# Kernel tuning notes

Hardware: AMD Instinct MI355X
Metric: run time of the kernel (lower is better)

Reference implementation:

```python
import jax, jax.numpy as jnp
import numpy as np

HEADS = 4
DIM_HEAD = 32


def _ln(x, g, b, eps=1e-5):
    m = x.mean(-1, keepdims=True)
    v = ((x - m) ** 2).mean(-1, keepdims=True)
    return (x - m) * jax.lax.rsqrt(v + eps) * g + b


def setup_inputs() -> dict:
    key = jax.random.key(0)
    B, N, D, H, W, h, w = 2, 6, 128, 50, 50, 14, 30
    HD = HEADS * DIM_HEAD  # 128
    ks = jax.random.split(key, 12)
    inp = {
        'q': jax.random.normal(ks[0], (B, N, D, H, W), jnp.float32),
        'k': jax.random.normal(ks[1], (B, N, D, h, w), jnp.float32),
        'v': jax.random.normal(ks[2], (B, N, D, h, w), jnp.float32),
        'skip': jax.random.normal(ks[3], (B, D, H, W), jnp.float32),
        # to_q / to_k / to_v: LayerNorm(dim) + Linear(dim, heads*dim_head)
        'lnq_g': jnp.ones((D,), jnp.float32), 'lnq_b': jnp.zeros((D,), jnp.float32),
        'wq': jax.random.normal(ks[4], (D, HD), jnp.float32) * 0.02,
        'bq': jnp.zeros((HD,), jnp.float32),
        'lnk_g': jnp.ones((D,), jnp.float32), 'lnk_b': jnp.zeros((D,), jnp.float32),
        'wk': jax.random.normal(ks[5], (D, HD), jnp.float32) * 0.02,
        'bk': jnp.zeros((HD,), jnp.float32),
        'lnv_g': jnp.ones((D,), jnp.float32), 'lnv_b': jnp.zeros((D,), jnp.float32),
        'wv': jax.random.normal(ks[6], (D, HD), jnp.float32) * 0.02,
        'bv': jnp.zeros((HD,), jnp.float32),
        # proj: Linear(heads*dim_head, dim)
        'wp': jax.random.normal(ks[7], (HD, D), jnp.float32) * 0.02,
        'bp': jnp.zeros((D,), jnp.float32),
        # prenorm
        'ln1_g': jnp.ones((D,), jnp.float32), 'ln1_b': jnp.zeros((D,), jnp.float32),
        # mlp: Linear(dim, 2*dim), GELU, Linear(2*dim, dim)
        'w1': jax.random.normal(ks[8], (D, 2 * D), jnp.float32) * 0.02,
        'b1': jnp.zeros((2 * D,), jnp.float32),
        'w2': jax.random.normal(ks[9], (2 * D, D), jnp.float32) * 0.02,
        'b2': jnp.zeros((D,), jnp.float32),
        # postnorm
        'ln2_g': jnp.ones((D,), jnp.float32), 'ln2_b': jnp.zeros((D,), jnp.float32),
    }
    return inp


def reference(q, k, v, skip,
              lnq_g, lnq_b, wq, bq,
              lnk_g, lnk_b, wk, bk,
              lnv_g, lnv_b, wv, bv,
              wp, bp, ln1_g, ln1_b,
              w1, b1, w2, b2, ln2_g, ln2_b):
    B, N, D, H, W = q.shape
    hk = k.shape[3] * k.shape[4]  # keys per camera
    Q = H * W
    M, DH = HEADS, DIM_HEAD
    scale = DH ** -0.5

    # (b n d H W) -> (b n Q d); (b n d h w) -> (b n K d); v -> (b (n K) d)
    qf = q.reshape(B, N, D, Q).transpose(0, 1, 3, 2)
    kf = k.reshape(B, N, D, hk).transpose(0, 1, 3, 2)
    vf = v.reshape(B, N, D, hk).transpose(0, 1, 3, 2).reshape(B, N * hk, D)

    qp = _ln(qf, lnq_g, lnq_b) @ wq + bq          # (B,N,Q,M*DH)
    kp = _ln(kf, lnk_g, lnk_b) @ wk + bk          # (B,N,K,M*DH)
    vp = _ln(vf, lnv_g, lnv_b) @ wv + bv          # (B,N*K,M*DH)

    qh = qp.reshape(B, N, Q, M, DH)
    kh = kp.reshape(B, N, hk, M, DH)
    vh = vp.reshape(B, N * hk, M, DH)

    # In the torch code only dot1+dot2 (queries from cameras 0 and 1) reach the
    # softmax; the q[:,1:]=... writes are no-ops and dot3..dot6 are unused.
    qsum = qh[:, 0] + qh[:, 1]                    # (B,Q,M,DH)
    dot = scale * jnp.einsum('bqmd,bnkmd->bmqnk', qsum, kh)  # (B,M,Q,N,K)
    dot = dot.reshape(B, M, Q, N * hk)
    att = jax.nn.softmax(dot, axis=-1)

    a = jnp.einsum('bmqk,bkmd->bqmd', att, vh).reshape(B, Q, M * DH)
    z = a @ wp + bp                               # (B,Q,D)
    z = z + skip.reshape(B, D, Q).transpose(0, 2, 1)
    z = _ln(z, ln1_g, ln1_b)
    z = z + (jax.nn.gelu(z @ w1 + b1, approximate=False) @ w2 + b2)
    z = _ln(z, ln2_g, ln2_b)
    return z.transpose(0, 2, 1).reshape(B, D, H, W)
```

## Files before the change

### kernel.cpp

```cpp
#include <hip/hip_runtime.h>
#include <hip/hip_bf16.h>
#include <math.h>

#define B_  2
#define N_  6
#define D_  128
#define Q_  2500
#define HK  420
#define NK  2520
#define NKP 2560
#define M_  4
#define DH  32
#define SPLIT 8
#define KPSP 320
#define CHUNKS 10
#define SCALE 0.25503487775f

typedef __attribute__((ext_vector_type(8))) short short8v;
typedef __attribute__((ext_vector_type(4))) float f32x4;
typedef __attribute__((ext_vector_type(2))) unsigned u32x2;
typedef __attribute__((ext_vector_type(4))) unsigned u32x4;

__device__ __forceinline__ unsigned short f2b(float x) {
  unsigned u = __float_as_uint(x);
  return (unsigned short)((u + 0x7FFFu + ((u >> 16) & 1u)) >> 16);
}

__device__ __forceinline__ unsigned pk2(float lo, float hi) {
  return (unsigned)f2b(lo) | ((unsigned)f2b(hi) << 16);
}

__device__ __forceinline__ float bl(unsigned u) { return __uint_as_float(u << 16); }
__device__ __forceinline__ float bh(unsigned u) { return __uint_as_float(u & 0xffff0000u); }

__device__ __forceinline__ int kperm(int a) {
  const int h = a & 7;
  return ((h >= 4) ? 16 : 0) + 4 * (a >> 3) + (h & 3);
}

__global__ __launch_bounds__(256)
void setup_kernel(const float* __restrict__ wp, const float* __restrict__ w1,
                  const float* __restrict__ w2, const float* __restrict__ wq,
                  const float* __restrict__ wk, const float* __restrict__ wv,
                  unsigned short* __restrict__ wpk, unsigned short* __restrict__ w1k,
                  unsigned short* __restrict__ w2k, unsigned short* __restrict__ wqk,
                  unsigned short* __restrict__ wkk, unsigned short* __restrict__ wvk,
                  unsigned short* __restrict__ kpb, unsigned short* __restrict__ vtb)
{
  if (blockIdx.x < 128) {
    const int base = blockIdx.x * 1024 + threadIdx.x * 4;
    #pragma unroll
    for (int i = 0; i < 4; ++i) {
      const int tid = base + i;
      if (tid < 16384) {
        const int e = tid & 7, l = (tid >> 3) & 63, j = (tid >> 9) & 7, c = tid >> 12;
        wpk[tid] = f2b(wp[(32*c + 8*(l>>4) + e) * 128 + 16*j + (l & 15)]);
      } else if (tid < 49152) {
        const int t2 = tid - 16384;
        const int e = t2 & 7, l = (t2 >> 3) & 63, j = (t2 >> 9) & 15, c = t2 >> 13;
        w1k[t2] = f2b(w1[(32*c + 8*(l>>4) + e) * 256 + 16*j + (l & 15)]);
      } else if (tid < 81920) {
        const int t2 = tid - 49152;
        const int e = t2 & 7, l = (t2 >> 3) & 63, j = (t2 >> 9) & 7, c = t2 >> 12;
        w2k[t2] = f2b(w2[(32*c + 8*(l>>4) + e) * 128 + 16*j + (l & 15)]);
      } else {
        const int t2 = (tid - 81920) & 16383;
        const int which = (tid - 81920) >> 14;
        const float* src = which == 0 ? wq : which == 1 ? wk : wv;
        unsigned short* dst = which == 0 ? wqk : which == 1 ? wkk : wvk;
        const int e = t2 & 7, l = (t2 >> 3) & 63, j = (t2 >> 9) & 7, c = t2 >> 12;
        dst[t2] = f2b(src[(32*c + 8*(l>>4) + e) * 128 + 16*j + (l & 15)]);
      }
    }
  } else {
    const int base = (blockIdx.x - 128) * 256 + threadIdx.x;
    for (int i = base; i < 16384; i += 512) {
      const int bm = i >> 11, rem = i & 2047;
      kpb[((size_t)bm * NKP + 2496 + (rem >> 5)) * DH + (rem & 31)] = 0;
      vtb[((size_t)(i >> 6)) * NKP + 2496 + (i & 63)] = 0;
    }
  }
}

__global__ __launch_bounds__(256)
void proj_kernel(const float* __restrict__ kin, const float* __restrict__ vin,
                 const float* __restrict__ lnk_g, const float* __restrict__ lnk_b,
                 const unsigned short* __restrict__ wkk, const float* __restrict__ bk,
                 const float* __restrict__ lnv_g, const float* __restrict__ lnv_b,
                 const unsigned short* __restrict__ wvk, const float* __restrict__ bv,
                 unsigned short* __restrict__ kpb, unsigned short* __restrict__ vtb,
                 const float* __restrict__ qin,
                 const float* __restrict__ lnq_g, const float* __restrict__ lnq_b,
                 const unsigned short* __restrict__ wqk, const float* __restrict__ bq,
                 unsigned short* __restrict__ qsb)
{
  const int wid = threadIdx.x >> 6, lane = threadIdx.x & 63;
  const int l15 = lane & 15, g = lane >> 4;

  if (blockIdx.x < 158) {
    const int T = blockIdx.x * 4 + wid;
    if (T >= 630) return;
    const int ph = T >= 315 ? 1 : 0;
    const int t = ph ? T - 315 : T;

    const float* in = ph ? vin : kin;
    const float* gg = ph ? lnv_g : lnk_g;
    const float* bb = ph ? lnv_b : lnk_b;
    const unsigned short* wf = ph ? wvk : wkk;
    const float* bs = ph ? bv : bk;

    const int myrow = 16 * t + l15;
    const int cam = myrow / HK, kk = myrow - cam * HK;

    float x[4][8];
    float s = 0.f, s2 = 0.f;
    #pragma unroll
    for (int c = 0; c < 4; ++c)
      #pragma unroll
      for (int e = 0; e < 8; ++e) {
        const float xv = in[((size_t)(cam * D_ + 32 * c + 8 * g + e)) * HK + kk];
        x[c][e] = xv; s += xv; s2 += xv * xv;
      }
    s  += __shfl_xor(s, 16);  s2 += __shfl_xor(s2, 16);
    s  += __shfl_xor(s, 32);  s2 += __shfl_xor(s2, 32);
    const float mean = s * (1.f / 128.f);
    const float rstd = rsqrtf(s2 * (1.f / 128.f) - mean * mean + 1e-5f);

    short8v aA[4];
    #pragma unroll
    for (int c = 0; c < 4; ++c)
      #pragma unroll
      for (int e = 0; e < 8; ++e) {
        const int col = 32 * c + 8 * g + e;
        aA[c][e] = (short)f2b((x[c][e] - mean) * rstd * gg[col] + bb[col]);
      }

    f32x4 z[8];
    #pragma unroll
    for (int j = 0; j < 8; ++j) {
      f32x4 d = {0.f, 0.f, 0.f, 0.f};
      #pragma unroll
      for (int c = 0; c < 4; ++c) {
        const short8v w8 = *(const short8v*)(wf + (((c * 8 + j) * 64 + lane) << 3));
        d = __builtin_amdgcn_mfma_f32_16x16x32_bf16(aA[c], w8, d, 0, 0, 0);
      }
      z[j] = d;
    }

    const int key0 = 16 * t + 4 * g;
    #pragma unroll
    for (int j = 0; j < 8; ++j) {
      const int col = 16 * j + l15;
      const float bsv = bs[col];
      if (ph == 0) {
        const int m = col >> 5, dh = col & 31;
        #pragma unroll
        for (int r = 0; r < 4; ++r) {
          const int key = key0 + r;
          const int bbx = key / NK, kb = key - bbx * NK;
          const int kbp = (kb & ~31) | kperm(kb & 31);
          kpb[((size_t)(bbx * M_ + m) * NKP + kbp) * DH + dh] = f2b(z[j][r] + bsv);
        }
      } else {
        #pragma unroll
        for (int r = 0; r < 4; ++r) {
          const int key = key0 + r;
          const int bbx = key / NK, kb = key - bbx * NK;
          vtb[((size_t)(bbx * 128 + col)) * NKP + kb] = f2b(z[j][r] + bsv);
        }
      }
    }
  } else {
    const int t = (blockIdx.x - 158) * 4 + wid;
    if (t >= 313) return;
    int myrow = 16 * t + l15; if (myrow > 4999) myrow = 4999;
    const int b = myrow / Q_, qpos = myrow - b * Q_;

    float xs[4][8];
    #pragma unroll
    for (int c = 0; c < 4; ++c)
      #pragma unroll
      for (int e = 0; e < 8; ++e) xs[c][e] = 0.f;

    #pragma unroll
    for (int n = 0; n < 2; ++n) {
      float x[4][8];
      float s = 0.f, s2 = 0.f;
      #pragma unroll
      for (int c = 0; c < 4; ++c)
        #pragma unroll
        for (int e = 0; e < 8; ++e) {
          const float xv = qin[((size_t)((b * N_ + n) * D_ + 32 * c + 8 * g + e)) * Q_ + qpos];
          x[c][e] = xv; s += xv; s2 += xv * xv;
        }
      s  += __shfl_xor(s, 16);  s2 += __shfl_xor(s2, 16);
      s  += __shfl_xor(s, 32);  s2 += __shfl_xor(s2, 32);
      const float mean = s * (1.f / 128.f);
      const float rstd = rsqrtf(s2 * (1.f / 128.f) - mean * mean + 1e-5f);
      #pragma unroll
      for (int c = 0; c < 4; ++c)
        #pragma unroll
        for (int e = 0; e < 8; ++e) xs[c][e] += (x[c][e] - mean) * rstd;
    }

    short8v aA[4];
    #pragma unroll
    for (int c = 0; c < 4; ++c) {
      #pragma unroll
      for (int e = 0; e < 8; ++e) {
        const int col = 32 * c + 8 * g + e;
        aA[c][e] = (short)f2b(SCALE * (xs[c][e] * lnq_g[col] + 2.f * lnq_b[col]));
      }
    }

    f32x4 z[8];
    #pragma unroll
    for (int j = 0; j < 8; ++j) {
      f32x4 d = {0.f, 0.f, 0.f, 0.f};
      #pragma unroll
      for (int c = 0; c < 4; ++c) {
        const short8v w8 = *(const short8v*)(wqk + (((c * 8 + j) * 64 + lane) << 3));
        d = __builtin_amdgcn_mfma_f32_16x16x32_bf16(aA[c], w8, d, 0, 0, 0);
      }
      z[j] = d;
    }

    const int row0 = 16 * t + 4 * g;
    #pragma unroll
    for (int j = 0; j < 8; ++j) {
      const int col = 16 * j + l15;
      const float bsv = 2.f * SCALE * bq[col];
      #pragma unroll
      for (int r = 0; r < 4; ++r) {
        const int row = row0 + r;
        if (row < 5000) qsb[((size_t)row) * 128 + col] = f2b(z[j][r] + bsv);
      }
    }
  }
}

__global__ __launch_bounds__(256)
void attn_kernel(const unsigned short* __restrict__ qsb,
                 const unsigned short* __restrict__ kpb,
                 const unsigned short* __restrict__ vtb,
                 float* __restrict__ pl, unsigned short* __restrict__ pacc)
{
  const int wid  = threadIdx.x >> 6;
  const int lane = threadIdx.x & 63;
  const int bi = blockIdx.x;
  const int sp = bi & 7;
  const int tmp = bi >> 3;
  const int qg = tmp % 20;
  const int bm = tmp / 20;
  const int qp = qg * 4 + wid;

  const int q16 = lane & 15, g = lane >> 4;
  const int qa = (2 * qp) * 16 + q16;
  const int qb = (2 * qp + 1) * 16 + q16;
  const int qca = qa < Q_ ? qa : Q_ - 1;
  const int qcb = qb < Q_ ? qb : Q_ - 1;
  const int b = bm >> 2;

  const short8v qf0 = *(const short8v*)(qsb + ((size_t)(b * Q_ + qca)) * 128 + (bm & 3) * DH + g * 8);
  const short8v qf1 = *(const short8v*)(qsb + ((size_t)(b * Q_ + qcb)) * 128 + (bm & 3) * DH + g * 8);

  const unsigned short* kbase = kpb + ((size_t)bm * NKP + sp * KPSP) * DH + q16 * DH + g * 8;
  const unsigned short* vbase = vtb + ((size_t)(bm * DH + q16)) * NKP + sp * KPSP + g * 8;

  f32x4 o0a = {0,0,0,0}, o1a = {0,0,0,0}, o0b = {0,0,0,0}, o1b = {0,0,0,0};
  float la = 0.f, lb = 0.f;

  const int c0 = qp % CHUNKS;
  int c1 = c0 + 1; if (c1 >= CHUNKS) c1 -= CHUNKS;
  int cn = c0 + 2; if (cn >= CHUNKS) cn -= CHUNKS;

  short8v kA1 = *(const short8v*)(kbase + c0 * 1024);
  short8v kA2 = *(const short8v*)(kbase + c0 * 1024 + 512);
  short8v vA1 = *(const short8v*)(vbase + c0 * 32);
  short8v vA2 = *(const short8v*)(vbase + c0 * 32 + 16 * NKP);
  short8v kB1 = *(const short8v*)(kbase + c1 * 1024);
  short8v kB2 = *(const short8v*)(kbase + c1 * 1024 + 512);
  short8v vB1 = *(const short8v*)(vbase + c1 * 32);
  short8v vB2 = *(const short8v*)(vbase + c1 * 32 + 16 * NKP);

  auto step = [&](short8v& K1r, short8v& K2r, short8v& V1r, short8v& V2r, int cnx) {
    f32x4 s0a = __builtin_amdgcn_mfma_f32_16x16x32_bf16(K1r, qf0, (f32x4){0.f,0.f,0.f,0.f}, 0, 0, 0);
    f32x4 s1a = __builtin_amdgcn_mfma_f32_16x16x32_bf16(K2r, qf0, (f32x4){0.f,0.f,0.f,0.f}, 0, 0, 0);
    f32x4 s0b = __builtin_amdgcn_mfma_f32_16x16x32_bf16(K1r, qf1, (f32x4){0.f,0.f,0.f,0.f}, 0, 0, 0);
    f32x4 s1b = __builtin_amdgcn_mfma_f32_16x16x32_bf16(K2r, qf1, (f32x4){0.f,0.f,0.f,0.f}, 0, 0, 0);

    float pa[8], pb_[8];
    #pragma unroll
    for (int r = 0; r < 4; ++r) {
      pa[r] = __builtin_amdgcn_exp2f(s0a[r]);  pa[4 + r] = __builtin_amdgcn_exp2f(s1a[r]);
      pb_[r] = __builtin_amdgcn_exp2f(s0b[r]); pb_[4 + r] = __builtin_amdgcn_exp2f(s1b[r]);
    }
    #pragma unroll
    for (int i = 0; i < 8; ++i) { la += pa[i]; lb += pb_[i]; }

    short8v fa, fb;
    #pragma unroll
    for (int i = 0; i < 8; ++i) { fa[i] = (short)f2b(pa[i]); fb[i] = (short)f2b(pb_[i]); }

    o0a = __builtin_amdgcn_mfma_f32_16x16x32_bf16(V1r, fa, o0a, 0, 0, 0);
    o1a = __builtin_amdgcn_mfma_f32_16x16x32_bf16(V2r, fa, o1a, 0, 0, 0);
    o0b = __builtin_amdgcn_mfma_f32_16x16x32_bf16(V1r, fb, o0b, 0, 0, 0);
    o1b = __builtin_amdgcn_mfma_f32_16x16x32_bf16(V2r, fb, o1b, 0, 0, 0);

    K1r = *(const short8v*)(kbase + cnx * 1024);
    K2r = *(const short8v*)(kbase + cnx * 1024 + 512);
    V1r = *(const short8v*)(vbase + cnx * 32);
    V2r = *(const short8v*)(vbase + cnx * 32 + 16 * NKP);
  };

  #pragma unroll 1
  for (int it = 0; it < CHUNKS / 2; ++it) {
    step(kA1, kA2, vA1, vA2, cn);
    cn = cn + 1 >= CHUNKS ? cn + 1 - CHUNKS : cn + 1;
    step(kB1, kB2, vB1, vB2, cn);
    cn = cn + 1 >= CHUNKS ? cn + 1 - CHUNKS : cn + 1;
  }

  la += __shfl_xor(la, 16);  la += __shfl_xor(la, 32);
  lb += __shfl_xor(lb, 16);  lb += __shfl_xor(lb, 32);

  if (qa < Q_) {
    const size_t row = (size_t)(bm * SPLIT + sp) * Q_ + qa;
    if (lane < 16) __builtin_nontemporal_store(la, &pl[row]);
    u32x2 w0, w1;
    w0[0] = pk2(o0a[0], o0a[1]); w0[1] = pk2(o0a[2], o0a[3]);
    w1[0] = pk2(o1a[0], o1a[1]); w1[1] = pk2(o1a[2], o1a[3]);
    __builtin_nontemporal_store(w0, (u32x2*)(pacc + row * DH + 4 * g));
    __builtin_nontemporal_store(w1, (u32x2*)(pacc + row * DH + 16 + 4 * g));
  }
  if (qb < Q_) {
    const size_t row = (size_t)(bm * SPLIT + sp) * Q_ + qb;
    if (lane < 16) __builtin_nontemporal_store(lb, &pl[row]);
    u32x2 w0, w1;
    w0[0] = pk2(o0b[0], o0b[1]); w0[1] = pk2(o0b[2], o0b[3]);
    w1[0] = pk2(o1b[0], o1b[1]); w1[1] = pk2(o1b[2], o1b[3]);
    __builtin_nontemporal_store(w0, (u32x2*)(pacc + row * DH + 4 * g));
    __builtin_nontemporal_store(w1, (u32x2*)(pacc + row * DH + 16 + 4 * g));
  }
}

__global__ __launch_bounds__(256)
void tail_kernel(const float* __restrict__ pl, const unsigned short* __restrict__ pacc,
                 const float* __restrict__ skip,
                 const unsigned short* __restrict__ wpk, const float* __restrict__ bp,
                 const float* __restrict__ ln1_g, const float* __restrict__ ln1_b,
                 const unsigned short* __restrict__ w1k, const float* __restrict__ b1,
                 const unsigned short* __restrict__ w2k, const float* __restrict__ b2,
                 const float* __restrict__ ln2_g, const float* __restrict__ ln2_b,
                 float* __restrict__ out)
{
  __shared__ __align__(16) unsigned short aL[16][136];
  __shared__ __align__(16) unsigned short zl[16][136];
  __shared__ __align__(16) unsigned short hl[16][264];
  __shared__ __align__(16) float stat1[4][16][2];
  __shared__ __align__(16) float stat2[4][16][2];

  const int wid = threadIdx.x >> 6, lane = threadIdx.x & 63;
  const int l15 = lane & 15, g = lane >> 4;
  const int row0 = blockIdx.x * 16;
  const int grow0 = row0 + 4 * g;

  {
    int arow = row0 + l15; if (arow > 4999) arow = 4999;
    const int bb = arow / Q_, qq = arow - bb * Q_;
    float ls = -40.0f;
    float4 a0 = {0,0,0,0}, a1 = {0,0,0,0};
    #pragma unroll
    for (int sp = 0; sp < SPLIT; ++sp) {
      const size_t row = (size_t)((bb * 4 + wid) * SPLIT + sp) * Q_ + qq;
      ls += __builtin_nontemporal_load(&pl[row]);
      const u32x4 t = __builtin_nontemporal_load((const u32x4*)(pacc + row * DH + 8 * g));
      a0.x += bl(t[0]); a0.y += bh(t[0]); a0.z += bl(t[1]); a0.w += bh(t[1]);
      a1.x += bl(t[2]); a1.y += bh(t[2]); a1.z += bl(t[3]); a1.w += bh(t[3]);
    }
    const float inv = 1.f / ls;
    u32x4 w;
    w[0] = pk2(a0.x * inv, a0.y * inv);
    w[1] = pk2(a0.z * inv, a0.w * inv);
    w[2] = pk2(a1.x * inv, a1.y * inv);
    w[3] = pk2(a1.z * inv, a1.w * inv);
    *(u32x4*)&aL[l15][32 * wid + 8 * g] = w;
  }
  __syncthreads();

  short8v aA[4];
  #pragma unroll
  for (int c = 0; c < 4; ++c)
    aA[c] = *(const short8v*)&aL[l15][32 * c + 8 * g];

  f32x4 zres[2];
  #pragma unroll
  for (int jj = 0; jj < 2; ++jj) {
    const int j = 2 * wid + jj;
    f32x4 d = {0.f, 0.f, 0.f, 0.f};
    #pragma unroll
    for (int c = 0; c < 4; ++c) {
      const short8v wf = *(const short8v*)(wpk + (((c * 8 + j) * 64 + lane) << 3));
      d = __builtin_amdgcn_mfma_f32_16x16x32_bf16(aA[c], wf, d, 0, 0, 0);
    }
    zres[jj] = d;
  }

  #pragma unroll
  for (int jj = 0; jj < 2; ++jj) {
    const int col = 16 * (2 * wid + jj) + l15;
    const float bpv = bp[col];
    #pragma unroll
    for (int r = 0; r < 4; ++r) {
      int rr = grow0 + r; if (rr > 4999) rr = 4999;
      const int bb = rr / 2500, q = rr - bb * 2500;
      zres[jj][r] += bpv + skip[((size_t)(bb * 128 + col)) * 2500 + q];
    }
  }

  {
    float sum[4], sq[4];
    #pragma unroll
    for (int r = 0; r < 4; ++r) {
      sum[r] = zres[0][r] + zres[1][r];
      sq[r]  = zres[0][r] * zres[0][r] + zres[1][r] * zres[1][r];
    }
    #pragma unroll
    for (int r = 0; r < 4; ++r) {
      #pragma unroll
      for (int off = 1; off < 16; off <<= 1) {
        sum[r] += __shfl_xor(sum[r], off);
        sq[r]  += __shfl_xor(sq[r], off);
      }
    }
    if (l15 == 0) {
      float4 s0 = {sum[0], sq[0], sum[1], sq[1]};
      float4 s1 = {sum[2], sq[2], sum[3], sq[3]};
      *(float4*)&stat1[wid][4 * g][0]     = s0;
      *(float4*)&stat1[wid][4 * g + 2][0] = s1;
    }
  }
  __syncthreads();

  float mean[4], rstd[4];
  #pragma unroll
  for (int r = 0; r < 4; ++r) {
    float S = 0.f, S2 = 0.f;
    #pragma unroll
    for (int w2 = 0; w2 < 4; ++w2) {
      S  += stat1[w2][4 * g + r][0];
      S2 += stat1[w2][4 * g + r][1];
    }
    mean[r] = S * (1.f / 128.f);
    rstd[r] = rsqrtf(S2 * (1.f / 128.f) - mean[r] * mean[r] + 1e-5f);
  }

  #pragma unroll
  for (int jj = 0; jj < 2; ++jj) {
    const int col = 16 * (2 * wid + jj) + l15;
    const float g1 = ln1_g[col], bv1 = ln1_b[col];
    #pragma unroll
    for (int r = 0; r < 4; ++r) {
      const float vv = (zres[jj][r] - mean[r]) * rstd[r] * g1 + bv1;
      zres[jj][r] = vv;
      zl[4 * g + r][col] = f2b(vv);
    }
  }
  __syncthreads();

  short8v zA[4];
  #pragma unroll
  for (int c = 0; c < 4; ++c)
    zA[c] = *(const short8v*)&zl[l15][32 * c + 8 * g];
  #pragma unroll
  for (int jj = 0; jj < 4; ++jj) {
    const int j = 4 * wid + jj;
    f32x4 d = {0.f, 0.f, 0.f, 0.f};
    #pragma unroll
    for (int c = 0; c < 4; ++c) {
      const short8v wf = *(const short8v*)(w1k + (((c * 16 + j) * 64 + lane) << 3));
      d = __builtin_amdgcn_mfma_f32_16x16x32_bf16(zA[c], wf, d, 0, 0, 0);
    }
    const int col = 16 * j + l15;
    const float bv = b1[col];
    #pragma unroll
    for (int r = 0; r < 4; ++r) {
      const float x = d[r] + bv;
      hl[4 * g + r][col] = f2b(0.5f * x * (1.f + erff(x * 0.70710678118654752f)));
    }
  }
  __syncthreads();

  short8v hA[8];
  #pragma unroll
  for (int c = 0; c < 8; ++c)
    hA[c] = *(const short8v*)&hl[l15][32 * c + 8 * g];
  #pragma unroll
  for (int jj = 0; jj < 2; ++jj) {
    const int j = 2 * wid + jj;
    f32x4 d = {0.f, 0.f, 0.f, 0.f};
    #pragma unroll
    for (int c = 0; c < 8; ++c) {
      const short8v wf = *(const short8v*)(w2k + (((c * 8 + j) * 64 + lane) << 3));
      d = __builtin_amdgcn_mfma_f32_16x16x32_bf16(hA[c], wf, d, 0, 0, 0);
    }
    const int col = 16 * j + l15;
    const float bv = b2[col];
    #pragma unroll
    for (int r = 0; r < 4; ++r) zres[jj][r] += d[r] + bv;
  }

  {
    float sum[4], sq[4];
    #pragma unroll
    for (int r = 0; r < 4; ++r) {
      sum[r] = zres[0][r] + zres[1][r];
      sq[r]  = zres[0][r] * zres[0][r] + zres[1][r] * zres[1][r];
    }
    #pragma unroll
    for (int r = 0; r < 4; ++r) {
      #pragma unroll
      for (int off = 1; off < 16; off <<= 1) {
        sum[r] += __shfl_xor(sum[r], off);
        sq[r]  += __shfl_xor(sq[r], off);
      }
    }
    if (l15 == 0) {
      float4 s0 = {sum[0], sq[0], sum[1], sq[1]};
      float4 s1 = {sum[2], sq[2], sum[3], sq[3]};
      *(float4*)&stat2[wid][4 * g][0]     = s0;
      *(float4*)&stat2[wid][4 * g + 2][0] = s1;
    }
  }
  __syncthreads();

  float mean2[4], rstd2[4];
  #pragma unroll
  for (int r = 0; r < 4; ++r) {
    float S = 0.f, S2 = 0.f;
    #pragma unroll
    for (int w2 = 0; w2 < 4; ++w2) {
      S  += stat2[w2][4 * g + r][0];
      S2 += stat2[w2][4 * g + r][1];
    }
    mean2[r] = S * (1.f / 128.f);
    rstd2[r] = rsqrtf(S2 * (1.f / 128.f) - mean2[r] * mean2[r] + 1e-5f);
  }

  if (grow0 + 3 <= 4999) {
    const int bb = grow0 / 2500, q0 = grow0 - bb * 2500;
    #pragma unroll
    for (int jj = 0; jj < 2; ++jj) {
      const int col = 16 * (2 * wid + jj) + l15;
      const float g2 = ln2_g[col], bv2 = ln2_b[col];
      float4 o;
      o.x = (zres[jj][0] - mean2[0]) * rstd2[0] * g2 + bv2;
      o.y = (zres[jj][1] - mean2[1]) * rstd2[1] * g2 + bv2;
      o.z = (zres[jj][2] - mean2[2]) * rstd2[2] * g2 + bv2;
      o.w = (zres[jj][3] - mean2[3]) * rstd2[3] * g2 + bv2;
      *(float4*)(out + ((size_t)(bb * 128 + col)) * 2500 + q0) = o;
    }
  }
}

extern "C" void kernel_launch(void* const* d_in, const int* in_sizes, int n_in,
                              void* d_out, int out_size, void* d_ws, size_t ws_size,
                              hipStream_t stream)
{
  const float* q     = (const float*)d_in[0];
  const float* k     = (const float*)d_in[1];
  const float* v     = (const float*)d_in[2];
  const float* skip  = (const float*)d_in[3];
  const float* lnq_g = (const float*)d_in[4];
  const float* lnq_b = (const float*)d_in[5];
  const float* wq    = (const float*)d_in[6];
  const float* bq    = (const float*)d_in[7];
  const float* lnk_g = (const float*)d_in[8];
  const float* lnk_b = (const float*)d_in[9];
  const float* wk    = (const float*)d_in[10];
  const float* bk    = (const float*)d_in[11];
  const float* lnv_g = (const float*)d_in[12];
  const float* lnv_b = (const float*)d_in[13];
  const float* wv    = (const float*)d_in[14];
  const float* bv    = (const float*)d_in[15];
  const float* wp    = (const float*)d_in[16];
  const float* bp    = (const float*)d_in[17];
  const float* ln1_g = (const float*)d_in[18];
  const float* ln1_b = (const float*)d_in[19];
  const float* w1    = (const float*)d_in[20];
  const float* b1    = (const float*)d_in[21];
  const float* w2    = (const float*)d_in[22];
  const float* b2    = (const float*)d_in[23];
  const float* ln2_g = (const float*)d_in[24];
  const float* ln2_b = (const float*)d_in[25];

  unsigned short* kpb = (unsigned short*)d_ws;
  unsigned short* vtb = kpb + 655360;
  unsigned short* qsb = vtb + 655360;
  unsigned short* wpk = qsb + 640000;
  unsigned short* w1k = wpk + 16384;
  unsigned short* w2k = w1k + 32768;
  unsigned short* wqk = w2k + 32768;
  unsigned short* wkk = wqk + 16384;
  unsigned short* wvk = wkk + 16384;
  float* pl = (float*)(wvk + 16384);
  unsigned short* pacc = (unsigned short*)(pl + 160000);

  setup_kernel<<<dim3(130), dim3(256), 0, stream>>>(wp, w1, w2, wq, wk, wv,
                                                    wpk, w1k, w2k, wqk, wkk, wvk,
                                                    kpb, vtb);
  proj_kernel<<<dim3(237), dim3(256), 0, stream>>>(
      k, v, lnk_g, lnk_b, wkk, bk, lnv_g, lnv_b, wvk, bv, kpb, vtb,
      q, lnq_g, lnq_b, wqk, bq, qsb);
  attn_kernel<<<dim3(1280), dim3(256), 0, stream>>>(qsb, kpb, vtb, pl, pacc);
  tail_kernel<<<dim3(313), dim3(256), 0, stream>>>(
      pl, pacc, skip, wpk, bp, ln1_g, ln1_b, w1k, b1, w2k, b2, ln2_g, ln2_b, (float*)d_out);
}
```

Measured before the change: 63.21 us.

## Process four query tiles per wave in attention to reuse K/V registers

Each wave in the attention kernel now handles four 16-query tiles instead of two, so every K and V fragment loaded from memory feeds twice as many MFMAs, and the grid is halved to match. The exp/pack step is also restructured to pack probability pairs straight into bf16 words and to issue the next K loads earlier within the step. The aim is to cut redundant K/V global loads per query. In exchange, register pressure rises with eight accumulators and four Q fragments, and there are fewer blocks to fill the GPU.

```diff
diff --git a/kernel.cpp b/kernel.cpp
--- a/kernel.cpp
+++ b/kernel.cpp
@@ -250,27 +250,39 @@
   const int bi = blockIdx.x;
   const int sp = bi & 7;
   const int tmp = bi >> 3;
-  const int qg = tmp % 20;
-  const int bm = tmp / 20;
-  const int qp = qg * 4 + wid;
+  const int qqg = tmp % 10;
+  const int bm = tmp / 10;
+  const int quad = qqg * 4 + wid;
 
   const int q16 = lane & 15, g = lane >> 4;
-  const int qa = (2 * qp) * 16 + q16;
-  const int qb = (2 * qp + 1) * 16 + q16;
-  const int qca = qa < Q_ ? qa : Q_ - 1;
-  const int qcb = qb < Q_ ? qb : Q_ - 1;
   const int b = bm >> 2;
 
-  const short8v qf0 = *(const short8v*)(qsb + ((size_t)(b * Q_ + qca)) * 128 + (bm & 3) * DH + g * 8);
-  const short8v qf1 = *(const short8v*)(qsb + ((size_t)(b * Q_ + qcb)) * 128 + (bm & 3) * DH + g * 8);
+  int qx[4];
+  short8v qf0, qf1, qf2, qf3;
+  {
+    #pragma unroll
+    for (int i = 0; i < 4; ++i) qx[i] = (4 * quad + i) * 16 + q16;
+    const int c0i = qx[0] < Q_ ? qx[0] : Q_ - 1;
+    const int c1i = qx[1] < Q_ ? qx[1] : Q_ - 1;
+    const int c2i = qx[2] < Q_ ? qx[2] : Q_ - 1;
+    const int c3i = qx[3] < Q_ ? qx[3] : Q_ - 1;
+    const size_t off = (bm & 3) * DH + g * 8;
+    qf0 = *(const short8v*)(qsb + ((size_t)(b * Q_ + c0i)) * 128 + off);
+    qf1 = *(const short8v*)(qsb + ((size_t)(b * Q_ + c1i)) * 128 + off);
+    qf2 = *(const short8v*)(qsb + ((size_t)(b * Q_ + c2i)) * 128 + off);
+    qf3 = *(const short8v*)(qsb + ((size_t)(b * Q_ + c3i)) * 128 + off);
+  }
 
   const unsigned short* kbase = kpb + ((size_t)bm * NKP + sp * KPSP) * DH + q16 * DH + g * 8;
   const unsigned short* vbase = vtb + ((size_t)(bm * DH + q16)) * NKP + sp * KPSP + g * 8;
 
-  f32x4 o0a = {0,0,0,0}, o1a = {0,0,0,0}, o0b = {0,0,0,0}, o1b = {0,0,0,0};
-  float la = 0.f, lb = 0.f;
-
-  const int c0 = qp % CHUNKS;
+  f32x4 o0_0 = {0,0,0,0}, o1_0 = {0,0,0,0};
+  f32x4 o0_1 = {0,0,0,0}, o1_1 = {0,0,0,0};
+  f32x4 o0_2 = {0,0,0,0}, o1_2 = {0,0,0,0};
+  f32x4 o0_3 = {0,0,0,0}, o1_3 = {0,0,0,0};
+  float l0 = 0.f, l1 = 0.f, l2 = 0.f, l3 = 0.f;
+
+  const int c0 = quad % CHUNKS;
   int c1 = c0 + 1; if (c1 >= CHUNKS) c1 -= CHUNKS;
   int cn = c0 + 2; if (cn >= CHUNKS) cn -= CHUNKS;
 
@@ -284,31 +296,50 @@
   short8v vB2 = *(const short8v*)(vbase + c1 * 32 + 16 * NKP);
 
   auto step = [&](short8v& K1r, short8v& K2r, short8v& V1r, short8v& V2r, int cnx) {
-    f32x4 s0a = __builtin_amdgcn_mfma_f32_16x16x32_bf16(K1r, qf0, (f32x4){0.f,0.f,0.f,0.f}, 0, 0, 0);
-    f32x4 s1a = __builtin_amdgcn_mfma_f32_16x16x32_bf16(K2r, qf0, (f32x4){0.f,0.f,0.f,0.f}, 0, 0, 0);
-    f32x4 s0b = __builtin_amdgcn_mfma_f32_16x16x32_bf16(K1r, qf1, (f32x4){0.f,0.f,0.f,0.f}, 0, 0, 0);
-    f32x4 s1b = __builtin_amdgcn_mfma_f32_16x16x32_bf16(K2r, qf1, (f32x4){0.f,0.f,0.f,0.f}, 0, 0, 0);
-
-    float pa[8], pb_[8];
-    #pragma unroll
-    for (int r = 0; r < 4; ++r) {
-      pa[r] = __builtin_amdgcn_exp2f(s0a[r]);  pa[4 + r] = __builtin_amdgcn_exp2f(s1a[r]);
-      pb_[r] = __builtin_amdgcn_exp2f(s0b[r]); pb_[4 + r] = __builtin_amdgcn_exp2f(s1b[r]);
-    }
-    #pragma unroll
-    for (int i = 0; i < 8; ++i) { la += pa[i]; lb += pb_[i]; }
-
-    short8v fa, fb;
-    #pragma unroll
-    for (int i = 0; i < 8; ++i) { fa[i] = (short)f2b(pa[i]); fb[i] = (short)f2b(pb_[i]); }
-
-    o0a = __builtin_amdgcn_mfma_f32_16x16x32_bf16(V1r, fa, o0a, 0, 0, 0);
-    o1a = __builtin_amdgcn_mfma_f32_16x16x32_bf16(V2r, fa, o1a, 0, 0, 0);
-    o0b = __builtin_amdgcn_mfma_f32_16x16x32_bf16(V1r, fb, o0b, 0, 0, 0);
-    o1b = __builtin_amdgcn_mfma_f32_16x16x32_bf16(V2r, fb, o1b, 0, 0, 0);
+    f32x4 s0_0 = __builtin_amdgcn_mfma_f32_16x16x32_bf16(K1r, qf0, (f32x4){0.f,0.f,0.f,0.f}, 0, 0, 0);
+    f32x4 s1_0 = __builtin_amdgcn_mfma_f32_16x16x32_bf16(K2r, qf0, (f32x4){0.f,0.f,0.f,0.f}, 0, 0, 0);
+    f32x4 s0_1 = __builtin_amdgcn_mfma_f32_16x16x32_bf16(K1r, qf1, (f32x4){0.f,0.f,0.f,0.f}, 0, 0, 0);
+    f32x4 s1_1 = __builtin_amdgcn_mfma_f32_16x16x32_bf16(K2r, qf1, (f32x4){0.f,0.f,0.f,0.f}, 0, 0, 0);
+    f32x4 s0_2 = __builtin_amdgcn_mfma_f32_16x16x32_bf16(K1r, qf2, (f32x4){0.f,0.f,0.f,0.f}, 0, 0, 0);
+    f32x4 s1_2 = __builtin_amdgcn_mfma_f32_16x16x32_bf16(K2r, qf2, (f32x4){0.f,0.f,0.f,0.f}, 0, 0, 0);
+    f32x4 s0_3 = __builtin_amdgcn_mfma_f32_16x16x32_bf16(K1r, qf3, (f32x4){0.f,0.f,0.f,0.f}, 0, 0, 0);
+    f32x4 s1_3 = __builtin_amdgcn_mfma_f32_16x16x32_bf16(K2r, qf3, (f32x4){0.f,0.f,0.f,0.f}, 0, 0, 0);
 
     K1r = *(const short8v*)(kbase + cnx * 1024);
     K2r = *(const short8v*)(kbase + cnx * 1024 + 512);
+
+    u32x4 u0, u1, u2, u3;
+    float p0, p1;
+    #pragma unroll
+    for (int j = 0; j < 4; ++j) {
+      const int r0 = 2 * j, r1 = 2 * j + 1;
+      const float a0 = __builtin_amdgcn_exp2f(j < 2 ? s0_0[r0] : s1_0[r0 - 4]);
+      const float a1 = __builtin_amdgcn_exp2f(j < 2 ? s0_0[r1] : s1_0[r1 - 4]);
+      l0 += a0 + a1; u0[j] = pk2(a0, a1);
+      const float b0 = __builtin_amdgcn_exp2f(j < 2 ? s0_1[r0] : s1_1[r0 - 4]);
+      const float b1 = __builtin_amdgcn_exp2f(j < 2 ? s0_1[r1] : s1_1[r1 - 4]);
+      l1 += b0 + b1; u1[j] = pk2(b0, b1);
+      const float cc0 = __builtin_amdgcn_exp2f(j < 2 ? s0_2[r0] : s1_2[r0 - 4]);
+      const float cc1 = __builtin_amdgcn_exp2f(j < 2 ? s0_2[r1] : s1_2[r1 - 4]);
+      l2 += cc0 + cc1; u2[j] = pk2(cc0, cc1);
+      const float d0 = __builtin_amdgcn_exp2f(j < 2 ? s0_3[r0] : s1_3[r0 - 4]);
+      const float d1 = __builtin_amdgcn_exp2f(j < 2 ? s0_3[r1] : s1_3[r1 - 4]);
+      l3 += d0 + d1; u3[j] = pk2(d0, d1);
+    }
+    const short8v f0 = __builtin_bit_cast(short8v, u0);
+    const short8v f1 = __builtin_bit_cast(short8v, u1);
+    const short8v f2 = __builtin_bit_cast(short8v, u2);
+    const short8v f3 = __builtin_bit_cast(short8v, u3);
+
+    o0_0 = __builtin_amdgcn_mfma_f32_16x16x32_bf16(V1r, f0, o0_0, 0, 0, 0);
+    o1_0 = __builtin_amdgcn_mfma_f32_16x16x32_bf16(V2r, f0, o1_0, 0, 0, 0);
+    o0_1 = __builtin_amdgcn_mfma_f32_16x16x32_bf16(V1r, f1, o0_1, 0, 0, 0);
+    o1_1 = __builtin_amdgcn_mfma_f32_16x16x32_bf16(V2r, f1, o1_1, 0, 0, 0);
+    o0_2 = __builtin_amdgcn_mfma_f32_16x16x32_bf16(V1r, f2, o0_2, 0, 0, 0);
+    o1_2 = __builtin_amdgcn_mfma_f32_16x16x32_bf16(V2r, f2, o1_2, 0, 0, 0);
+    o0_3 = __builtin_amdgcn_mfma_f32_16x16x32_bf16(V1r, f3, o0_3, 0, 0, 0);
+    o1_3 = __builtin_amdgcn_mfma_f32_16x16x32_bf16(V2r, f3, o1_3, 0, 0, 0);
+
     V1r = *(const short8v*)(vbase + cnx * 32);
     V2r = *(const short8v*)(vbase + cnx * 32 + 16 * NKP);
   };
@@ -321,26 +352,26 @@
     cn = cn + 1 >= CHUNKS ? cn + 1 - CHUNKS : cn + 1;
   }
 
-  la += __shfl_xor(la, 16);  la += __shfl_xor(la, 32);
-  lb += __shfl_xor(lb, 16);  lb += __shfl_xor(lb, 32);
-
-  if (qa < Q_) {
-    const size_t row = (size_t)(bm * SPLIT + sp) * Q_ + qa;
-    if (lane < 16) __builtin_nontemporal_store(la, &pl[row]);
-    u32x2 w0, w1;
-    w0[0] = pk2(o0a[0], o0a[1]); w0[1] = pk2(o0a[2], o0a[3]);
-    w1[0] = pk2(o1a[0], o1a[1]); w1[1] = pk2(o1a[2], o1a[3]);
-    __builtin_nontemporal_store(w0, (u32x2*)(pacc + row * DH + 4 * g));
-    __builtin_nontemporal_store(w1, (u32x2*)(pacc + row * DH + 16 + 4 * g));
-  }
-  if (qb < Q_) {
-    const size_t row = (size_t)(bm * SPLIT + sp) * Q_ + qb;
-    if (lane < 16) __builtin_nontemporal_store(lb, &pl[row]);
-    u32x2 w0, w1;
-    w0[0] = pk2(o0b[0], o0b[1]); w0[1] = pk2(o0b[2], o0b[3]);
-    w1[0] = pk2(o1b[0], o1b[1]); w1[1] = pk2(o1b[2], o1b[3]);
-    __builtin_nontemporal_store(w0, (u32x2*)(pacc + row * DH + 4 * g));
-    __builtin_nontemporal_store(w1, (u32x2*)(pacc + row * DH + 16 + 4 * g));
+  l0 += __shfl_xor(l0, 16);  l0 += __shfl_xor(l0, 32);
+  l1 += __shfl_xor(l1, 16);  l1 += __shfl_xor(l1, 32);
+  l2 += __shfl_xor(l2, 16);  l2 += __shfl_xor(l2, 32);
+  l3 += __shfl_xor(l3, 16);  l3 += __shfl_xor(l3, 32);
+
+  const size_t rbase = (size_t)(bm * SPLIT + sp) * Q_;
+  #pragma unroll
+  for (int i = 0; i < 4; ++i) {
+    const f32x4 oo0 = i == 0 ? o0_0 : i == 1 ? o0_1 : i == 2 ? o0_2 : o0_3;
+    const f32x4 oo1 = i == 0 ? o1_0 : i == 1 ? o1_1 : i == 2 ? o1_2 : o1_3;
+    const float ll  = i == 0 ? l0 : i == 1 ? l1 : i == 2 ? l2 : l3;
+    if (qx[i] < Q_) {
+      const size_t row = rbase + qx[i];
+      if (lane < 16) __builtin_nontemporal_store(ll, &pl[row]);
+      u32x2 w0, w1;
+      w0[0] = pk2(oo0[0], oo0[1]); w0[1] = pk2(oo0[2], oo0[3]);
+      w1[0] = pk2(oo1[0], oo1[1]); w1[1] = pk2(oo1[2], oo1[3]);
+      __builtin_nontemporal_store(w0, (u32x2*)(pacc + row * DH + 4 * g));
+      __builtin_nontemporal_store(w1, (u32x2*)(pacc + row * DH + 16 + 4 * g));
+    }
   }
 }
 
@@ -612,7 +643,7 @@
   proj_kernel<<<dim3(237), dim3(256), 0, stream>>>(
       k, v, lnk_g, lnk_b, wkk, bk, lnv_g, lnv_b, wvk, bv, kpb, vtb,
       q, lnq_g, lnq_b, wqk, bq, qsb);
-  attn_kernel<<<dim3(1280), dim3(256), 0, stream>>>(qsb, kpb, vtb, pl, pacc);
+  attn_kernel<<<dim3(640), dim3(256), 0, stream>>>(qsb, kpb, vtb, pl, pacc);
   tail_kernel<<<dim3(313), dim3(256), 0, stream>>>(
       pl, pacc, skip, wpk, bp, ln1_g, ln1_b, w1k, b1, w2k, b2, ln2_g, ln2_b, (float*)d_out);
 }
```

Measured after the change: 58.94 us. -6.8%, faster.
